# Kernel optimization log

Hardware: AMD Instinct MI355X
Metric: run time of the kernel (lower is better)

The kernel has to match this reference:

```python
import jax, jax.numpy as jnp
import numpy as np

EPS = 1e-5

def setup_inputs() -> dict:
    key = jax.random.key(0)
    ks = jax.random.split(key, 10)
    B, C, H, W = 4, 512, 56, 56
    n_heads = 8
    nq = H * W
    oq = (H // 2) * (W // 2)  # sr_ratio=2, k=3,s=2,p=1 -> halved spatial dims
    s = 0.02
    return {
        'x': jax.random.normal(ks[0], (B, C, H, W), jnp.float32),
        'attn_weights': jax.random.uniform(ks[1], (B, n_heads, nq, oq), jnp.float32),
        'q_w': jax.random.normal(ks[2], (C, C), jnp.float32) * s,
        'k_w': jax.random.normal(ks[3], (C, C), jnp.float32) * s,
        'v_w': jax.random.normal(ks[4], (C, C), jnp.float32) * s,
        'sr_w': jax.random.normal(ks[5], (C, 1, 3, 3), jnp.float32) * s,  # depthwise OIHW
        'sr_b': jnp.zeros((C,), jnp.float32),
        'ln_g': jnp.ones((C,), jnp.float32),
        'ln_b': jnp.zeros((C,), jnp.float32),
        'tc_w': jax.random.normal(ks[6], (n_heads, n_heads), jnp.float32) * 0.3,  # 1x1 conv over heads
        'tc_b': jnp.zeros((n_heads,), jnp.float32),
        'proj_w': jax.random.normal(ks[7], (C, C), jnp.float32) * s,
        'proj_b': jnp.zeros((C,), jnp.float32),
    }

def _layernorm(x, g, b):
    m = jnp.mean(x, axis=-1, keepdims=True)
    v = jnp.var(x, axis=-1, keepdims=True)
    return (x - m) * jax.lax.rsqrt(v + EPS) * g + b

def reference(x, attn_weights, q_w, k_w, v_w, sr_w, sr_b, ln_g, ln_b, tc_w, tc_b, proj_w, proj_b):
    B, C, H, W = x.shape
    n_heads = tc_w.shape[0]
    hd = C // n_heads
    scale = hd ** -0.5
    nq = H * W
    xf = x.reshape(B, C, nq).transpose(0, 2, 1)  # (B, nq, C)
    q = (xf @ q_w.T).reshape(B, nq, n_heads, hd).transpose(0, 2, 1, 3)  # (B, h, nq, hd)
    # spatial reduction: depthwise conv k=3, s=2, p=1 on NCHW, then LayerNorm
    xs = jax.lax.conv_general_dilated(
        x, sr_w, window_strides=(2, 2), padding=((1, 1), (1, 1)),
        feature_group_count=C, dimension_numbers=('NCHW', 'OIHW', 'NCHW'))
    xs = xs + sr_b[None, :, None, None]
    oq = xs.shape[2] * xs.shape[3]
    xs = xs.reshape(B, C, oq).transpose(0, 2, 1)  # (B, oq, C)
    xs = _layernorm(xs, ln_g, ln_b)
    k = (xs @ k_w.T).reshape(B, oq, n_heads, hd).transpose(0, 2, 3, 1)  # (B, h, hd, oq)
    v = (xs @ v_w.T).reshape(B, oq, n_heads, hd).transpose(0, 2, 1, 3)  # (B, h, oq, hd)
    attn = jnp.einsum('bhqd,bhdo->bhqo', q, k) * scale  # (B, h, nq, oq)
    # apply_transform: 1x1 conv mixing heads -> softmax -> InstanceNorm2d (no affine)
    attn = jnp.einsum('bhqo,gh->bgqo', attn, tc_w) + tc_b[None, :, None, None]
    attn = jax.nn.softmax(attn, axis=-1)
    m = jnp.mean(attn, axis=(2, 3), keepdims=True)
    var = jnp.var(attn, axis=(2, 3), keepdims=True)
    attn = (attn - m) * jax.lax.rsqrt(var + EPS)
    attn = attn_weights * attn
    out = jnp.einsum('bhqo,bhod->bhqd', attn, v)  # (B, h, nq, hd)
    out = out.transpose(0, 2, 1, 3).reshape(B, nq, C)
    out = out @ proj_w.T + proj_b
    return out.reshape(B, H, W, C).transpose(0, 3, 1, 2)
```

## Files before the change

### kernel.cpp

```cpp
#include <hip/hip_runtime.h>

typedef _Float16 half8 __attribute__((ext_vector_type(8)));
typedef _Float16 half4 __attribute__((ext_vector_type(4)));
typedef float fx4 __attribute__((ext_vector_type(4)));

#define MFMA16(a,b,c) __builtin_amdgcn_mfma_f32_16x16x32_f16(a,b,c,0,0,0)

#define BN 4
#define CC 512
#define HH 56
#define WW 56
#define NQ 3136
#define OQ 784
#define NH 8
#define HD 64
#define NSEG 7
#define BGN (BN * NH * NQ)

__device__ inline half8 h8z() {
    half8 v;
#pragma unroll
    for (int j = 0; j < 8; j++) v[j] = (_Float16)0.f;
    return v;
}

__device__ __forceinline__ void glds16(const void* g, void* l) {
    __builtin_amdgcn_global_load_lds(
        (__attribute__((address_space(1))) const unsigned int*)g,
        (__attribute__((address_space(3))) unsigned int*)l, 16, 0, 0);
}

__global__ void cvt4_kernel(const float* __restrict__ a, const float* __restrict__ b,
                            const float* __restrict__ c, const float* __restrict__ d,
                            _Float16* __restrict__ o, float* __restrict__ S2) {
    if (blockIdx.x == 0 && blockIdx.y == 0 && threadIdx.x < 32) S2[threadIdx.x] = 0.f;
    int y = blockIdx.y;
    const float* s = (y == 0) ? a : (y == 1) ? b : (y == 2) ? c : d;
    int i = blockIdx.x * 256 + threadIdx.x;
    o[(size_t)y * 262144 + i] = (_Float16)s[i];
}

__global__ void xpose_kernel(const float* __restrict__ x, _Float16* __restrict__ xf) {
    __shared__ float t[32][33];
    int n0 = blockIdx.x * 32, c0 = blockIdx.y * 32, b = blockIdx.z;
    int tx = threadIdx.x, ty = threadIdx.y;
#pragma unroll
    for (int i = 0; i < 4; i++)
        t[ty + 8 * i][tx] = x[((size_t)(b * CC) + c0 + ty + 8 * i) * NQ + n0 + tx];
    __syncthreads();
#pragma unroll
    for (int i = 0; i < 4; i++)
        xf[((size_t)(b * NQ) + n0 + ty + 8 * i) * CC + c0 + tx] = (_Float16)t[tx][ty + 8 * i];
}

__global__ void dw_kernel(const float* __restrict__ x, const float* __restrict__ w,
                          const float* __restrict__ bias, float* __restrict__ xsc) {
    int cb = blockIdx.x, oy = blockIdx.y, b = blockIdx.z;
    int tx = threadIdx.x, ty = threadIdx.y;
    int c = cb * 16 + ty;
    float a = bias[c];
    const float* xp = x + ((size_t)(b * CC + c) * HH) * WW;
#pragma unroll
    for (int ky = 0; ky < 3; ky++) {
        int iy = 2 * oy - 1 + ky;
        if (iy < 0 || iy >= HH) continue;
#pragma unroll
        for (int kx = 0; kx < 3; kx++) {
            int ix = 2 * tx - 1 + kx;
            if (ix < 0 || ix >= WW) continue;
            a += xp[iy * WW + ix] * w[c * 9 + ky * 3 + kx];
        }
    }
    __shared__ float tile[28][17];
    tile[tx][ty] = a;
    __syncthreads();
    int lin = ty * 28 + tx;
    int oi = lin >> 4, ci = lin & 15;
    xsc[((size_t)(b * OQ) + oy * 28 + oi) * CC + cb * 16 + ci] = tile[oi][ci];
}

__global__ __launch_bounds__(256) void ln_kernel(const float* __restrict__ xsc,
        const float* __restrict__ g, const float* __restrict__ bb,
        _Float16* __restrict__ xs16) {
    int row = blockIdx.x;
    const float* rp = xsc + (size_t)row * CC;
    int t = threadIdx.x;
    float v0 = rp[t], v1 = rp[t + 256];
    float s = v0 + v1, ss = v0 * v0 + v1 * v1;
#pragma unroll
    for (int m = 1; m < 64; m <<= 1) {
        s += __shfl_xor(s, m, 64);
        ss += __shfl_xor(ss, m, 64);
    }
    __shared__ float red[8];
    int wv = t >> 6;
    if ((t & 63) == 0) { red[wv] = s; red[4 + wv] = ss; }
    __syncthreads();
    s = red[0] + red[1] + red[2] + red[3];
    ss = red[4] + red[5] + red[6] + red[7];
    float mean = s * (1.f / 512.f);
    float var = ss * (1.f / 512.f) - mean * mean;
    float rs = rsqrtf(var + 1e-5f);
    xs16[(size_t)row * CC + t] = (_Float16)((v0 - mean) * rs * g[t] + bb[t]);
    xs16[(size_t)row * CC + t + 256] = (_Float16)((v1 - mean) * rs * g[t + 256] + bb[t + 256]);
}

__global__ __launch_bounds__(256) void gemm_qkv(const _Float16* __restrict__ xf,
        const _Float16* __restrict__ xs, const _Float16* __restrict__ w4,
        _Float16* __restrict__ q16, _Float16* __restrict__ k16, _Float16* __restrict__ vT) {
    const int which = blockIdx.z;
    if (which && blockIdx.x >= 49) return;
    const _Float16* A = which ? xs : xf;
    const _Float16* Bw = w4 + (size_t)which * 262144;
    __shared__ _Float16 As[2][64 * 64];
    __shared__ _Float16 Bs[2][64 * 64];
    const int m0 = blockIdx.x * 64, n0 = blockIdx.y * 64;
    const int tid = threadIdx.x;
    const int lane = tid & 63, wv = tid >> 6;
    const int wm = (wv >> 1) * 32, wn = (wv & 1) * 32;
    const int l15 = lane & 15, quad = lane >> 4;
    fx4 acc[2][2];
#pragma unroll
    for (int i = 0; i < 2; i++)
#pragma unroll
        for (int j = 0; j < 2; j++) acc[i][j] = fx4{0.f, 0.f, 0.f, 0.f};

#define STAGEG(bf, kk)                                                       \
    {                                                                        \
        _Pragma("unroll") for (int i = 0; i < 2; i++) {                      \
            int id = tid + 256 * i;                                          \
            int r = id >> 3, gg = id & 7;                                    \
            int gs = gg ^ (r & 7);                                           \
            glds16(A + (size_t)(m0 + r) * 512 + (kk) + gs * 8,               \
                   &As[bf][(id & ~63) * 8]);                                 \
            glds16(Bw + (size_t)(n0 + r) * 512 + (kk) + gs * 8,              \
                   &Bs[bf][(id & ~63) * 8]);                                 \
        }                                                                    \
    }

    STAGEG(0, 0);
    __syncthreads();
    for (int kt = 0; kt < 8; kt++) {
        const int cur = kt & 1;
        if (kt < 7) STAGEG(cur ^ 1, (kt + 1) * 64);
#pragma unroll
        for (int ks = 0; ks < 2; ks++) {
            half8 af[2], bf[2];
#pragma unroll
            for (int s = 0; s < 2; s++) {
                int ra = wm + s * 16 + l15;
                int rb = wn + s * 16 + l15;
                af[s] = *(const half8*)(&As[cur][ra * 64 + ((ks * 4 + quad) ^ (ra & 7)) * 8]);
                bf[s] = *(const half8*)(&Bs[cur][rb * 64 + ((ks * 4 + quad) ^ (rb & 7)) * 8]);
            }
#pragma unroll
            for (int i = 0; i < 2; i++)
#pragma unroll
                for (int j = 0; j < 2; j++)
                    acc[i][j] = MFMA16(af[i], bf[j], acc[i][j]);
        }
        __syncthreads();
    }
#undef STAGEG

    if (which < 2) {
        _Float16* O = which ? k16 : q16;
#pragma unroll
        for (int i = 0; i < 2; i++)
#pragma unroll
            for (int j = 0; j < 2; j++) {
                int col = n0 + wn + j * 16 + l15;
#pragma unroll
                for (int e = 0; e < 4; e++) {
                    int row = m0 + wm + i * 16 + quad * 4 + e;
                    O[(size_t)row * 512 + col] = (_Float16)acc[i][j][e];
                }
            }
    } else {
#pragma unroll
        for (int i = 0; i < 2; i++) {
            int row = m0 + wm + i * 16 + quad * 4;
            int b = row / OQ;
            int o = row - b * OQ;
#pragma unroll
            for (int j = 0; j < 2; j++) {
                int c = n0 + wn + j * 16 + l15;
                half4 pk;
#pragma unroll
                for (int e = 0; e < 4; e++) pk[e] = (_Float16)acc[i][j][e];
                *(half4*)(vT + ((size_t)(b * NH + (c >> 6)) * HD + (c & 63)) * OQ + o) = pk;
            }
        }
    }
}

__global__ __launch_bounds__(256) void qk_mix(const _Float16* __restrict__ q16,
        const _Float16* __restrict__ k16, const float* __restrict__ tcw,
        const float* __restrict__ tcb, _Float16* __restrict__ L,
        float* __restrict__ Zpart, float* __restrict__ E2part) {
    __shared__ _Float16 kl[2][16 * 512];
    __shared__ float tcs[64];
    __shared__ float tbb[8];
    const int b = blockIdx.z, oseg = blockIdx.y, ob = oseg * 112;
    const int tid = threadIdx.x;
    const int wv = tid >> 6, lane = tid & 63, l15 = lane & 15, quad = lane >> 4;
    const int n0 = blockIdx.x * 64 + wv * 16;
    if (tid < 64) tcs[tid] = tcw[tid] * 0.125f;
    else if (tid < 72) tbb[tid - 64] = tcb[tid - 64];

    half8 aF[8][2];
    const _Float16* qrow = q16 + ((size_t)(b * NQ + n0 + l15)) * 512;
#pragma unroll
    for (int h = 0; h < 8; h++)
#pragma unroll
        for (int ks = 0; ks < 2; ks++)
            aF[h][ks] = *(const half8*)(qrow + h * 64 + ks * 32 + quad * 8);

    float z[8][4], s2[8][4];
#pragma unroll
    for (int g = 0; g < 8; g++)
#pragma unroll
        for (int e = 0; e < 4; e++) { z[g][e] = 0.f; s2[g][e] = 0.f; }

#define STAGEK(bf, oo)                                                       \
    {                                                                        \
        const _Float16* kbp = k16 + ((size_t)(b * OQ + (oo))) * 512;         \
        _Pragma("unroll") for (int i = 0; i < 4; i++) {                      \
            int id = tid + 256 * i;                                          \
            int r = id >> 6, g16 = id & 63;                                  \
            int gs = (g16 & 56) | ((g16 & 7) ^ (r & 7));                     \
            glds16(kbp + (size_t)r * 512 + gs * 8, &kl[bf][(id & ~63) * 8]); \
        }                                                                    \
    }

    STAGEK(0, ob);
    __syncthreads();

    for (int ot = 0; ot < 7; ot++) {
        const int cur = ot & 1;
        if (ot < 6) STAGEK(cur ^ 1, ob + (ot + 1) * 16);
        int o0 = ob + ot * 16;
        fx4 s[8];
#pragma unroll
        for (int h = 0; h < 8; h++) {
            fx4 a = fx4{0.f, 0.f, 0.f, 0.f};
#pragma unroll
            for (int ks = 0; ks < 2; ks++) {
                int colg = h * 8 + ks * 4 + quad;
                int rg = (colg & 56) | ((colg & 7) ^ (l15 & 7));
                half8 bF = *(const half8*)(&kl[cur][l15 * 512 + rg * 8]);
                a = MFMA16(aF[h][ks], bF, a);
            }
            s[h] = a;
        }
#pragma unroll
        for (int g = 0; g < 8; g++) {
            size_t tb = (((size_t)(b * 8 + g) * 196 + (n0 >> 4)) * 49 + (o0 >> 4)) * 256
                        + (l15 >> 3) * 128 + (l15 & 7);
#pragma unroll
            for (int e = 0; e < 4; e++) {
                float v = tbb[g];
#pragma unroll
                for (int h = 0; h < 8; h++) v += tcs[g * 8 + h] * s[h][e];
                _Float16 vh = (_Float16)v;
                float vr = (float)vh;
                float ex = __expf(vr);
                z[g][e] += ex;
                s2[g][e] += ex * ex;
                L[tb + (quad * 4 + e) * 8] = vh;
            }
        }
        __syncthreads();
    }
#undef STAGEK

#pragma unroll
    for (int m = 1; m < 16; m <<= 1) {
#pragma unroll
        for (int g = 0; g < 8; g++)
#pragma unroll
            for (int e = 0; e < 4; e++) {
                z[g][e] += __shfl_xor(z[g][e], m, 64);
                s2[g][e] += __shfl_xor(s2[g][e], m, 64);
            }
    }
    if (l15 < 8) {
        int g = l15;
        size_t base = (size_t)oseg * BGN + (size_t)(b * 8 + g) * NQ + n0 + quad * 4;
#pragma unroll
        for (int e = 0; e < 4; e++) {
            Zpart[base + e] = z[g][e];
            E2part[base + e] = s2[g][e];
        }
    }
}

__global__ __launch_bounds__(256) void zfin_kernel(const float* __restrict__ Zpart,
        const float* __restrict__ E2part, float* __restrict__ Zinv, float* __restrict__ S2) {
    int i = blockIdx.x * 256 + threadIdx.x;
    float z = 0.f, e2 = 0.f;
#pragma unroll
    for (int s = 0; s < NSEG; s++) {
        z += Zpart[(size_t)s * BGN + i];
        e2 += E2part[(size_t)s * BGN + i];
    }
    float zi = 1.f / z;
    Zinv[i] = zi;
    float r = e2 * zi * zi;
#pragma unroll
    for (int m = 1; m < 64; m <<= 1) r += __shfl_xor(r, m, 64);
    if ((threadIdx.x & 63) == 0) atomicAdd(&S2[i / NQ], r);
}

__global__ __launch_bounds__(256) void pv_kernel(const _Float16* __restrict__ Lt,
        const float* __restrict__ W, const _Float16* __restrict__ vT,
        const float* __restrict__ Zinv, const float* __restrict__ S2,
        _Float16* __restrict__ outp) {
    __shared__ float Ws[4][2][16 * 70];
    const int b = blockIdx.z, g = blockIdx.y;
    const int tid = threadIdx.x;
    const int wv = tid >> 6, lane = tid & 63, l15 = lane & 15, quad = lane >> 4;
    const int n0 = blockIdx.x * 64 + wv * 16;
    const int bg = b * 8 + g;
    const float mm = 1.f / (float)OQ;
    const float rv = rsqrtf(S2[bg] * (1.f / ((float)NQ * (float)OQ)) - mm * mm + 1e-5f);
    const float czr = Zinv[bg * NQ + n0 + l15] * rv;
    const float rm = rv * mm;
    const _Float16* Lb = Lt + (((size_t)bg * 196 + (n0 >> 4)) * 49) * 256 + lane * 8;
    const float* Wg = W + ((size_t)bg * NQ + n0 + (lane >> 4)) * OQ + (lane & 15) * 4;
    const float* Wrow = W + ((size_t)bg * NQ + n0 + l15) * OQ;
    const _Float16* vb = vT + (size_t)bg * HD * OQ + (size_t)l15 * OQ;
    float* WsW = &Ws[wv][0][0];
    const float* WsR = &Ws[wv][0][0] + l15 * 70 + quad * 8;

    fx4 wreg[4];
    half8 lA, lB, vA0, vA1, vA2, vA3, vB0, vB1, vB2, vB3;
    fx4 acc0 = fx4{0.f, 0.f, 0.f, 0.f};
    fx4 acc1 = fx4{0.f, 0.f, 0.f, 0.f};
    fx4 acc2 = fx4{0.f, 0.f, 0.f, 0.f};
    fx4 acc3 = fx4{0.f, 0.f, 0.f, 0.f};

#define LOADWG(g2)                                                           \
    {                                                                        \
        _Pragma("unroll") for (int i = 0; i < 4; i++)                        \
            wreg[i] = *(const fx4*)(Wg + (size_t)(4 * i) * OQ + (g2) * 64);  \
    }
#define DSWR(ph)                                                             \
    {                                                                        \
        _Pragma("unroll") for (int i = 0; i < 4; i++)                        \
            *(fx4*)(WsW + (ph) * (16 * 70) + ((lane >> 4) + 4 * i) * 70 +    \
                    (lane & 15) * 4) = wreg[i];                              \
    }
#define LOADL(c, d)                                                          \
    {                                                                        \
        if ((c) < 24 || lane < 32) d = *(const half8*)(Lb + (c) * 512);      \
        else d = h8z();                                                      \
    }
#define LOADV(c, d0, d1, d2, d3)                                             \
    {                                                                        \
        int kb = (c) * 32 + quad * 8;                                        \
        if (kb < OQ) {                                                       \
            d0 = *(const half8*)(vb + (size_t)(0 * 16) * OQ + kb);           \
            d1 = *(const half8*)(vb + (size_t)(1 * 16) * OQ + kb);           \
            d2 = *(const half8*)(vb + (size_t)(2 * 16) * OQ + kb);           \
            d3 = *(const half8*)(vb + (size_t)(3 * 16) * OQ + kb);           \
        } else { d0 = h8z(); d1 = h8z(); d2 = h8z(); d3 = h8z(); }           \
    }
#define COMPUTE_W(sL, wf0, wf1, s0, s1, s2, s3)                              \
    {                                                                        \
        half8 aH;                                                            \
        _Pragma("unroll") for (int j = 0; j < 8; j++) {                      \
            float e = __expf((float)sL[j]);                                  \
            float a = e * czr - rm;                                          \
            float wx = (j < 4) ? wf0[j] : wf1[j - 4];                        \
            aH[j] = (_Float16)(a * wx);                                      \
        }                                                                    \
        acc0 = MFMA16(aH, s0, acc0);                                         \
        acc1 = MFMA16(aH, s1, acc1);                                         \
        acc2 = MFMA16(aH, s2, acc2);                                         \
        acc3 = MFMA16(aH, s3, acc3);                                         \
    }

    LOADWG(0);
    LOADL(0, lA);
    LOADV(0, vA0, vA1, vA2, vA3);
    DSWR(0);
    LOADWG(1);

#pragma unroll 1
    for (int pi = 0; pi < 12; ++pi) {
        const int phC = pi & 1, phN = phC ^ 1;
        if (pi <= 10) DSWR(phN);
        if (pi <= 9) LOADWG(pi + 2);
        const int c0 = 2 * pi;
        LOADL(c0 + 1, lB);
        LOADV(c0 + 1, vB0, vB1, vB2, vB3);
        {
            const float* wr = WsR + phC * (16 * 70);
            fx4 wf0 = *(const fx4*)(wr);
            fx4 wf1 = *(const fx4*)(wr + 4);
            COMPUTE_W(lA, wf0, wf1, vA0, vA1, vA2, vA3);
        }
        LOADL(c0 + 2, lA);
        LOADV(c0 + 2, vA0, vA1, vA2, vA3);
        {
            const float* wr = WsR + phC * (16 * 70) + 32;
            fx4 wf0 = *(const fx4*)(wr);
            fx4 wf1 = *(const fx4*)(wr + 4);
            COMPUTE_W(lB, wf0, wf1, vB0, vB1, vB2, vB3);
        }
    }
    {
        fx4 wt0 = fx4{0.f, 0.f, 0.f, 0.f};
        fx4 wt1 = fx4{0.f, 0.f, 0.f, 0.f};
        int kb = 768 + quad * 8;
        if (kb < OQ) {
            wt0 = *(const fx4*)(Wrow + kb);
            wt1 = *(const fx4*)(Wrow + kb + 4);
        }
        COMPUTE_W(lA, wt0, wt1, vA0, vA1, vA2, vA3);
    }
#undef LOADWG
#undef DSWR
#undef LOADL
#undef LOADV
#undef COMPUTE_W

    fx4 acc[4] = {acc0, acc1, acc2, acc3};
#pragma unroll
    for (int ds = 0; ds < 4; ds++)
#pragma unroll
        for (int e = 0; e < 4; e++) {
            int n = n0 + quad * 4 + e;
            int c = g * 64 + ds * 16 + l15;
            outp[((size_t)b * NQ + n) * 512 + c] = (_Float16)acc[ds][e];
        }
}

__global__ __launch_bounds__(256) void gemm_proj(const _Float16* __restrict__ A,
        const _Float16* __restrict__ Ball, const float* __restrict__ bias,
        float* __restrict__ Oall) {
    __shared__ _Float16 As[2][64 * 64];
    __shared__ _Float16 Bs[2][64 * 64];
    const int b = blockIdx.z;
    const _Float16* Bm = Ball + (size_t)b * NQ * 512;
    float* O = Oall + (size_t)b * CC * NQ;
    const int m0 = blockIdx.x * 64, n0 = blockIdx.y * 64;
    const int tid = threadIdx.x;
    const int lane = tid & 63, wv = tid >> 6;
    const int wm = (wv >> 1) * 32, wn = (wv & 1) * 32;
    const int l15 = lane & 15, quad = lane >> 4;
    fx4 acc[2][2];
#pragma unroll
    for (int i = 0; i < 2; i++)
#pragma unroll
        for (int j = 0; j < 2; j++) acc[i][j] = fx4{0.f, 0.f, 0.f, 0.f};

#define STAGEP(bf, kk)                                                       \
    {                                                                        \
        _Pragma("unroll") for (int i = 0; i < 2; i++) {                      \
            int id = tid + 256 * i;                                          \
            int r = id >> 3, gg = id & 7;                                    \
            int gs = gg ^ (r & 7);                                           \
            glds16(A + (size_t)(m0 + r) * 512 + (kk) + gs * 8,               \
                   &As[bf][(id & ~63) * 8]);                                 \
            glds16(Bm + (size_t)(n0 + r) * 512 + (kk) + gs * 8,              \
                   &Bs[bf][(id & ~63) * 8]);                                 \
        }                                                                    \
    }

    STAGEP(0, 0);
    __syncthreads();
    for (int kt = 0; kt < 8; kt++) {
        const int cur = kt & 1;
        if (kt < 7) STAGEP(cur ^ 1, (kt + 1) * 64);
#pragma unroll
        for (int ks = 0; ks < 2; ks++) {
            half8 af[2], bf[2];
#pragma unroll
            for (int s = 0; s < 2; s++) {
                int ra = wm + s * 16 + l15;
                int rb = wn + s * 16 + l15;
                af[s] = *(const half8*)(&As[cur][ra * 64 + ((ks * 4 + quad) ^ (ra & 7)) * 8]);
                bf[s] = *(const half8*)(&Bs[cur][rb * 64 + ((ks * 4 + quad) ^ (rb & 7)) * 8]);
            }
#pragma unroll
            for (int i = 0; i < 2; i++)
#pragma unroll
                for (int j = 0; j < 2; j++)
                    acc[i][j] = MFMA16(af[i], bf[j], acc[i][j]);
        }
        __syncthreads();
    }
#undef STAGEP

#pragma unroll
    for (int i = 0; i < 2; i++)
#pragma unroll
        for (int j = 0; j < 2; j++) {
            int col = n0 + wn + j * 16 + l15;
#pragma unroll
            for (int e = 0; e < 4; e++) {
                int row = m0 + wm + i * 16 + quad * 4 + e;
                O[(size_t)row * NQ + col] = acc[i][j][e] + bias[row];
            }
        }
}

extern "C" void kernel_launch(void* const* d_in, const int* in_sizes, int n_in,
                              void* d_out, int out_size, void* d_ws, size_t ws_size,
                              hipStream_t stream) {
    const float* x = (const float*)d_in[0];
    const float* aw = (const float*)d_in[1];
    const float* q_w = (const float*)d_in[2];
    const float* k_w = (const float*)d_in[3];
    const float* v_w = (const float*)d_in[4];
    const float* sr_w = (const float*)d_in[5];
    const float* sr_b = (const float*)d_in[6];
    const float* ln_g = (const float*)d_in[7];
    const float* ln_b = (const float*)d_in[8];
    const float* tc_w = (const float*)d_in[9];
    const float* tc_b = (const float*)d_in[10];
    const float* p_w = (const float*)d_in[11];
    const float* p_b = (const float*)d_in[12];
    float* out = (float*)d_out;

    char* p = (char*)d_ws;
    auto take = [&](size_t bytes) -> char* {
        char* r = p;
        p += (bytes + 255) & ~(size_t)255;
        return r;
    };
    _Float16* qw16 = (_Float16*)take(512 * 512 * 2);
    _Float16* kw16 = (_Float16*)take(512 * 512 * 2);
    _Float16* vw16 = (_Float16*)take(512 * 512 * 2);
    _Float16* pw16 = (_Float16*)take(512 * 512 * 2);
    _Float16* xf16 = (_Float16*)take((size_t)BN * NQ * CC * 2);
    float* xsc = (float*)take((size_t)BN * OQ * CC * 4);
    _Float16* xs16 = (_Float16*)take((size_t)BN * OQ * CC * 2);
    _Float16* q16 = (_Float16*)take((size_t)BN * NQ * CC * 2);
    _Float16* k16 = (_Float16*)take((size_t)BN * OQ * CC * 2);
    _Float16* vT = (_Float16*)take((size_t)BN * OQ * CC * 2);
    _Float16* outp = (_Float16*)take((size_t)BN * NQ * CC * 2);
    float* Zpart = (float*)take((size_t)NSEG * BGN * 4);
    float* E2part = (float*)take((size_t)NSEG * BGN * 4);
    float* S2 = (float*)take(32 * 4);
    float* Zinv = (float*)take((size_t)BGN * 4);
    _Float16* L = (_Float16*)take((size_t)BN * NH * NQ * OQ * 2);

    cvt4_kernel<<<dim3(1024, 4), 256, 0, stream>>>(q_w, k_w, v_w, p_w, qw16, S2);
    xpose_kernel<<<dim3(98, 16, BN), dim3(32, 8), 0, stream>>>(x, xf16);
    dw_kernel<<<dim3(32, 28, BN), dim3(28, 16), 0, stream>>>(x, sr_w, sr_b, xsc);
    ln_kernel<<<BN * OQ, 256, 0, stream>>>(xsc, ln_g, ln_b, xs16);
    gemm_qkv<<<dim3(196, 8, 3), 256, 0, stream>>>(xf16, xs16, qw16, q16, k16, vT);
    qk_mix<<<dim3(49, 7, BN), 256, 0, stream>>>(q16, k16, tc_w, tc_b, L, Zpart, E2part);
    zfin_kernel<<<BGN / 256, 256, 0, stream>>>(Zpart, E2part, Zinv, S2);
    pv_kernel<<<dim3(49, 8, BN), 256, 0, stream>>>(L, aw, vT, Zinv, S2, outp);
    gemm_proj<<<dim3(8, 49, BN), 256, 0, stream>>>(pw16, outp, p_b, out);
}
```

Measured before the change: 706.9 us.

## Deepen L prefetch, remap block order, and use nontemporal loads in pv_kernel

Double-buffers the L-tile loads two chunks ahead using a ping-pong register array and fully unrolls the main loop so more loads are in flight. Remaps the block index so the 8 heads of the same batch and row block are scheduled adjacently, which can improve cache reuse of shared data. Marks the streaming W and L loads as nontemporal to reduce cache pollution. Full unrolling and the extra buffers raise register pressure and code size, which could lower occupancy.

```diff
diff --git a/kernel.cpp b/kernel.cpp
--- a/kernel.cpp
+++ b/kernel.cpp
@@ -317,10 +317,14 @@
         const float* __restrict__ Zinv, const float* __restrict__ S2,
         _Float16* __restrict__ outp) {
     __shared__ float Ws[4][2][16 * 70];
-    const int b = blockIdx.z, g = blockIdx.y;
+    const int f = blockIdx.x + 49 * (blockIdx.y + 8 * blockIdx.z);
+    const int g = f & 7;
+    const int r = f >> 3;
+    const int b = r & 3;
+    const int nblk = r >> 2;
     const int tid = threadIdx.x;
     const int wv = tid >> 6, lane = tid & 63, l15 = lane & 15, quad = lane >> 4;
-    const int n0 = blockIdx.x * 64 + wv * 16;
+    const int n0 = nblk * 64 + wv * 16;
     const int bg = b * 8 + g;
     const float mm = 1.f / (float)OQ;
     const float rv = rsqrtf(S2[bg] * (1.f / ((float)NQ * (float)OQ)) - mm * mm + 1e-5f);
@@ -334,7 +338,9 @@
     const float* WsR = &Ws[wv][0][0] + l15 * 70 + quad * 8;
 
     fx4 wreg[4];
-    half8 lA, lB, vA0, vA1, vA2, vA3, vB0, vB1, vB2, vB3;
+    half8 lq[2][2];
+    half8 vE0, vE1, vE2, vE3;
+    half8 vO0, vO1, vO2, vO3;
     fx4 acc0 = fx4{0.f, 0.f, 0.f, 0.f};
     fx4 acc1 = fx4{0.f, 0.f, 0.f, 0.f};
     fx4 acc2 = fx4{0.f, 0.f, 0.f, 0.f};
@@ -343,7 +349,8 @@
 #define LOADWG(g2)                                                           \
     {                                                                        \
         _Pragma("unroll") for (int i = 0; i < 4; i++)                        \
-            wreg[i] = *(const fx4*)(Wg + (size_t)(4 * i) * OQ + (g2) * 64);  \
+            wreg[i] = __builtin_nontemporal_load(                            \
+                (const fx4*)(Wg + (size_t)(4 * i) * OQ + (g2) * 64));        \
     }
 #define DSWR(ph)                                                             \
     {                                                                        \
@@ -353,7 +360,8 @@
     }
 #define LOADL(c, d)                                                          \
     {                                                                        \
-        if ((c) < 24 || lane < 32) d = *(const half8*)(Lb + (c) * 512);      \
+        if ((c) < 25 && ((c) < 24 || lane < 32))                             \
+            d = __builtin_nontemporal_load((const half8*)(Lb + (size_t)(c) * 512)); \
         else d = h8z();                                                      \
     }
 #define LOADV(c, d0, d1, d2, d3)                                             \
@@ -381,33 +389,33 @@
         acc3 = MFMA16(aH, s3, acc3);                                         \
     }
 
+    LOADL(0, lq[0][0]);
+    LOADL(1, lq[0][1]);
     LOADWG(0);
-    LOADL(0, lA);
-    LOADV(0, vA0, vA1, vA2, vA3);
+    LOADV(0, vE0, vE1, vE2, vE3);
     DSWR(0);
     LOADWG(1);
 
-#pragma unroll 1
+#pragma unroll
     for (int pi = 0; pi < 12; ++pi) {
-        const int phC = pi & 1, phN = phC ^ 1;
-        if (pi <= 10) DSWR(phN);
+        const int pc = pi & 1, pn = pc ^ 1;
+        LOADL(2 * pi + 2, lq[pn][0]);
+        LOADL(2 * pi + 3, lq[pn][1]);
+        if (pi <= 10) DSWR(pn);
         if (pi <= 9) LOADWG(pi + 2);
-        const int c0 = 2 * pi;
-        LOADL(c0 + 1, lB);
-        LOADV(c0 + 1, vB0, vB1, vB2, vB3);
+        LOADV(2 * pi + 1, vO0, vO1, vO2, vO3);
         {
-            const float* wr = WsR + phC * (16 * 70);
+            const float* wr = WsR + pc * (16 * 70);
             fx4 wf0 = *(const fx4*)(wr);
             fx4 wf1 = *(const fx4*)(wr + 4);
-            COMPUTE_W(lA, wf0, wf1, vA0, vA1, vA2, vA3);
-        }
-        LOADL(c0 + 2, lA);
-        LOADV(c0 + 2, vA0, vA1, vA2, vA3);
+            COMPUTE_W(lq[pc][0], wf0, wf1, vE0, vE1, vE2, vE3);
+        }
+        LOADV(2 * pi + 2, vE0, vE1, vE2, vE3);
         {
-            const float* wr = WsR + phC * (16 * 70) + 32;
+            const float* wr = WsR + pc * (16 * 70) + 32;
             fx4 wf0 = *(const fx4*)(wr);
             fx4 wf1 = *(const fx4*)(wr + 4);
-            COMPUTE_W(lB, wf0, wf1, vB0, vB1, vB2, vB3);
+            COMPUTE_W(lq[pc][1], wf0, wf1, vO0, vO1, vO2, vO3);
         }
     }
     {
@@ -415,10 +423,10 @@
         fx4 wt1 = fx4{0.f, 0.f, 0.f, 0.f};
         int kb = 768 + quad * 8;
         if (kb < OQ) {
-            wt0 = *(const fx4*)(Wrow + kb);
-            wt1 = *(const fx4*)(Wrow + kb + 4);
-        }
-        COMPUTE_W(lA, wt0, wt1, vA0, vA1, vA2, vA3);
+            wt0 = __builtin_nontemporal_load((const fx4*)(Wrow + kb));
+            wt1 = __builtin_nontemporal_load((const fx4*)(Wrow + kb + 4));
+        }
+        COMPUTE_W(lq[0][0], wt0, wt1, vE0, vE1, vE2, vE3);
     }
 #undef LOADWG
 #undef DSWR
```

New measurement: 684.9 us. 3.1% less time.
